# Performance work log

Measured on AMD Instinct MI355X. Metric: run time of the kernel, lower is better.

## Reference

```python
import jax, jax.numpy as jnp
import numpy as np

B, T, HID, OUT = 32, 2048, 1024, 1024
DV = 1024
NEG_INF = jnp.float32(-jnp.inf)


def setup_inputs() -> dict:
    key = jax.random.key(0)
    ks = jax.random.split(key, 10)
    hidden = jax.random.normal(ks[0], (B, HID), dtype=jnp.float32)
    enc_key = jax.random.normal(ks[1], (B, T, OUT), dtype=jnp.float32)
    value = jax.random.normal(ks[2], (B, T, DV), dtype=jnp.float32)
    seq_lens = jnp.maximum(jax.random.randint(ks[3], (B,), 0, T), 1).astype(jnp.int32)
    # learned parameters (PyTorch Linear: y = x @ W.T + b; we store W already transposed)
    s_q = 1.0 / np.sqrt(HID)
    s_1 = 1.0 / np.sqrt(OUT)
    s_2 = 1.0 / np.sqrt(OUT // 2)
    Wq = jax.random.uniform(ks[4], (HID, OUT), minval=-s_q, maxval=s_q, dtype=jnp.float32)
    bq = jax.random.uniform(ks[5], (OUT,), minval=-s_q, maxval=s_q, dtype=jnp.float32)
    W1 = jax.random.uniform(ks[6], (OUT, OUT // 2), minval=-s_1, maxval=s_1, dtype=jnp.float32)
    b1 = jax.random.uniform(ks[7], (OUT // 2,), minval=-s_1, maxval=s_1, dtype=jnp.float32)
    W2 = jax.random.uniform(ks[8], (OUT // 2, 1), minval=-s_2, maxval=s_2, dtype=jnp.float32)
    b2 = jax.random.uniform(ks[9], (1,), minval=-s_2, maxval=s_2, dtype=jnp.float32)
    return {"hidden": hidden, "key": enc_key, "value": value, "seq_lens": seq_lens,
            "Wq": Wq, "bq": bq, "W1": W1, "b1": b1, "W2": W2, "b2": b2}


def reference(hidden, key, value, seq_lens, Wq, bq, W1, b1, W2, b2):
    # query projection: [B, OUT]
    query = hidden @ Wq + bq
    # additive Bahdanau: tanh(key + query) -> [B, T, OUT]
    h = jnp.tanh(key + query[:, None, :])
    # 2-layer score MLP (dropout p=0.2 is identity in eval mode)
    h = h @ W1 + b1                      # [B, T, OUT//2]
    scores = (h @ W2 + b2)[..., 0]       # [B, T]
    # mask positions >= seq_len with -inf, then softmax over T
    pos = jnp.arange(scores.shape[1])
    scores = jnp.where(pos[None, :] < seq_lens[:, None], scores, NEG_INF)
    attn = jax.nn.softmax(scores, axis=-1)  # [B, T]
    # context = attn @ value -> [B, DV]
    context = jnp.einsum('bt,btd->bd', attn, value)
    return (context, attn)
```

## Files before the change

### kernel.cpp

```cpp
#include <hip/hip_runtime.h>
#include <math.h>

#define BB 32
#define TT 2048
#define DD 1024
#define HF 512

#define QKS 64
#define QCH (DD / QKS)

#define CHK 32
#define NCH (TT / CHK)

__device__ __forceinline__ float tanh_fast(float x) {
    float e = __expf(2.0f * x);
    return 1.0f - 2.0f / (e + 1.0f);
}

__global__ void __launch_bounds__(256) prep_query_kernel(
        const float* __restrict__ hidden, const float* __restrict__ Wq,
        const float* __restrict__ W1, const float* __restrict__ b1,
        const float* __restrict__ W2, const float* __restrict__ b2,
        float* __restrict__ w, float* __restrict__ cbias,
        float* __restrict__ qpart) {
    __shared__ float smem[BB * QCH];
    int bx  = blockIdx.x;
    int tid = threadIdx.x;

    if (bx < 4) {
        int d = bx * 256 + tid;
        const float* row = W1 + (size_t)d * HF;
        float acc = 0.0f;
        #pragma unroll 8
        for (int j = 0; j < HF; j += 4) {
            float4 a = *(const float4*)(row + j);
            float4 b = *(const float4*)(W2 + j);
            acc += a.x * b.x + a.y * b.y + a.z * b.z + a.w * b.w;
        }
        w[d] = acc;
        return;
    }
    if (bx == 4) {
        __shared__ float red[256];
        float s = b1[tid] * W2[tid] + b1[tid + 256] * W2[tid + 256];
        red[tid] = s;
        __syncthreads();
        for (int off = 128; off; off >>= 1) {
            if (tid < off) red[tid] += red[tid + off];
            __syncthreads();
        }
        if (tid == 0) cbias[0] = red[0] + b2[0];
        return;
    }
    int idx = bx - 5, otile = idx & 3, ks = idx >> 2;
    int o = otile * 256 + tid, h0 = ks * QCH;
    if (tid < 128) {
        int r = tid >> 2, c4 = (tid & 3) << 2;
        *(float4*)&smem[r * QCH + c4] = *(const float4*)&hidden[(size_t)r * DD + h0 + c4];
    }
    __syncthreads();

    float wv[QCH];
    #pragma unroll
    for (int h = 0; h < QCH; ++h)
        wv[h] = Wq[(size_t)(h0 + h) * DD + o];

    float acc[BB];
    #pragma unroll
    for (int b = 0; b < BB; ++b) acc[b] = 0.0f;
    #pragma unroll
    for (int h = 0; h < QCH; ++h) {
        #pragma unroll
        for (int b = 0; b < BB; ++b)
            acc[b] = fmaf(smem[b * QCH + h], wv[h], acc[b]);
    }
    #pragma unroll
    for (int b = 0; b < BB; ++b)
        qpart[((size_t)ks * BB + b) * DD + o] = acc[b];
}

__global__ void __launch_bounds__(256) qreduce_kernel(
        const float* __restrict__ qpart, const float* __restrict__ bq,
        float* __restrict__ query) {
    int i = blockIdx.x * 256 + threadIdx.x;
    int o = i & (DD - 1);
    float a0 = bq[o], a1 = 0.0f, a2 = 0.0f, a3 = 0.0f;
    #pragma unroll 4
    for (int ks = 0; ks < QKS; ks += 4) {
        a0 += qpart[(size_t)(ks + 0) * (BB * DD) + i];
        a1 += qpart[(size_t)(ks + 1) * (BB * DD) + i];
        a2 += qpart[(size_t)(ks + 2) * (BB * DD) + i];
        a3 += qpart[(size_t)(ks + 3) * (BB * DD) + i];
    }
    query[i] = (a0 + a1) + (a2 + a3);
}

__global__ void __launch_bounds__(256, 8) score_ctx_kernel(
        const float* __restrict__ key, const float* __restrict__ value,
        const float* __restrict__ query, const float* __restrict__ w,
        const float* __restrict__ cb, const int* __restrict__ seq_lens,
        float* __restrict__ escore, float* __restrict__ psum,
        float* __restrict__ partial) {
    int item = blockIdx.x;
    int b    = item & (BB - 1);
    int x    = item >> 5;
    int len  = seq_lens[b];
    int t0   = x * CHK;
    if (t0 >= len) return;

    __shared__ float wsh[DD];
    __shared__ float qsh[DD];
    __shared__ float esm[CHK];
    int tid = threadIdx.x;
    { int i4 = tid * 4;
      *(float4*)&wsh[i4] = *(const float4*)&w[i4];
      *(float4*)&qsh[i4] = *(const float4*)&query[(size_t)b * DD + i4]; }
    __syncthreads();

    int wave = tid >> 6, lane = tid & 63;
    float c0 = cb[0];

    #pragma unroll 4
    for (int tt = 0; tt < CHK / 4; ++tt) {
        int r = tt * 4 + wave;
        int t = t0 + r;
        float e = 0.0f;
        if (t < len) {
            const float* krow = key + ((size_t)b * TT + t) * DD;
            float acc = 0.0f;
            #pragma unroll
            for (int kb = 0; kb < 4; ++kb) {
                int d = kb * 256 + lane * 4;
                float4 kv = *(const float4*)(krow + d);
                float4 qv = *(const float4*)&qsh[d];
                float4 wv = *(const float4*)&wsh[d];
                acc += tanh_fast(kv.x + qv.x) * wv.x;
                acc += tanh_fast(kv.y + qv.y) * wv.y;
                acc += tanh_fast(kv.z + qv.z) * wv.z;
                acc += tanh_fast(kv.w + qv.w) * wv.w;
            }
            #pragma unroll
            for (int off = 32; off; off >>= 1) acc += __shfl_down(acc, off);
            if (lane == 0) e = __expf(acc + c0);
        }
        if (lane == 0) esm[r] = e;
    }
    __syncthreads();

    if (tid < CHK) escore[(size_t)b * TT + t0 + tid] = esm[tid];
    if (tid == 0) {
        float s = 0.0f;
        #pragma unroll
        for (int i = 0; i < CHK; ++i) s += esm[i];
        psum[b * NCH + x] = s;
    }

    int d4 = tid * 4;
    int tend = min(t0 + CHK, len);
    const float* vbase = value + (size_t)b * TT * DD + d4;
    float4 acc0 = {0.0f, 0.0f, 0.0f, 0.0f};
    float4 acc1 = {0.0f, 0.0f, 0.0f, 0.0f};
    int t = t0;
    for (; t + 1 < tend; t += 2) {
        float a0 = esm[t - t0], a1 = esm[t - t0 + 1];
        float4 v0 = *(const float4*)(vbase + (size_t)t * DD);
        float4 v1 = *(const float4*)(vbase + (size_t)(t + 1) * DD);
        acc0.x = fmaf(a0, v0.x, acc0.x);  acc1.x = fmaf(a1, v1.x, acc1.x);
        acc0.y = fmaf(a0, v0.y, acc0.y);  acc1.y = fmaf(a1, v1.y, acc1.y);
        acc0.z = fmaf(a0, v0.z, acc0.z);  acc1.z = fmaf(a1, v1.z, acc1.z);
        acc0.w = fmaf(a0, v0.w, acc0.w);  acc1.w = fmaf(a1, v1.w, acc1.w);
    }
    if (t < tend) {
        float a0 = esm[t - t0];
        float4 v0 = *(const float4*)(vbase + (size_t)t * DD);
        acc0.x = fmaf(a0, v0.x, acc0.x);
        acc0.y = fmaf(a0, v0.y, acc0.y);
        acc0.z = fmaf(a0, v0.z, acc0.z);
        acc0.w = fmaf(a0, v0.w, acc0.w);
    }
    acc0.x += acc1.x; acc0.y += acc1.y; acc0.z += acc1.z; acc0.w += acc1.w;
    *(float4*)&partial[((size_t)(b * NCH + x)) * DD + d4] = acc0;
}

__global__ void __launch_bounds__(256) finalize_kernel(
        const float* __restrict__ partial, const float* __restrict__ escore,
        const float* __restrict__ psum, const int* __restrict__ seq_lens,
        float* __restrict__ ctx, float* __restrict__ attn) {
    __shared__ float red[NCH];
    int bx = blockIdx.x, tid = threadIdx.x;
    int b  = (bx < 128) ? (bx >> 2) : (((bx - 128) * 1024) >> 11);
    int len = seq_lens[b];
    int nch = (len + CHK - 1) / CHK;

    if (tid < NCH) red[tid] = (tid < nch) ? psum[b * NCH + tid] : 0.0f;
    __syncthreads();
    for (int off = NCH / 2; off; off >>= 1) {
        if (tid < off) red[tid] += red[tid + off];
        __syncthreads();
    }
    float Sinv = 1.0f / red[0];

    if (bx < 128) {
        int d = (bx & 3) * 256 + tid;
        const float* pb = partial + (size_t)b * NCH * DD + d;
        float a0 = 0.0f, a1 = 0.0f, a2 = 0.0f, a3 = 0.0f;
        int c = 0;
        for (; c + 3 < nch; c += 4) {
            a0 += pb[(size_t)(c + 0) * DD];
            a1 += pb[(size_t)(c + 1) * DD];
            a2 += pb[(size_t)(c + 2) * DD];
            a3 += pb[(size_t)(c + 3) * DD];
        }
        for (; c < nch; ++c) a0 += pb[(size_t)c * DD];
        ctx[(size_t)b * DD + d] = ((a0 + a1) + (a2 + a3)) * Sinv;
    } else {
        int idx = (bx - 128) * 1024 + tid * 4;
        int t   = idx & (TT - 1);
        float4 e = *(const float4*)&escore[(size_t)b * TT + t];
        float4 o;
        o.x = (t + 0 < len) ? e.x * Sinv : 0.0f;
        o.y = (t + 1 < len) ? e.y * Sinv : 0.0f;
        o.z = (t + 2 < len) ? e.z * Sinv : 0.0f;
        o.w = (t + 3 < len) ? e.w * Sinv : 0.0f;
        *(float4*)&attn[(size_t)b * TT + t] = o;
    }
}

extern "C" void kernel_launch(void* const* d_in, const int* in_sizes, int n_in,
                              void* d_out, int out_size, void* d_ws, size_t ws_size,
                              hipStream_t stream) {
    const float* hidden   = (const float*)d_in[0];
    const float* key      = (const float*)d_in[1];
    const float* value    = (const float*)d_in[2];
    const int*   seq_lens = (const int*)  d_in[3];
    const float* Wq       = (const float*)d_in[4];
    const float* bq       = (const float*)d_in[5];
    const float* W1       = (const float*)d_in[6];
    const float* b1       = (const float*)d_in[7];
    const float* W2       = (const float*)d_in[8];
    const float* b2       = (const float*)d_in[9];

    float* out  = (float*)d_out;
    float* ctx  = out;
    float* attn = out + BB * DD;

    float* ws      = (float*)d_ws;
    float* w       = ws;
    float* cb      = ws + 1024;
    float* query   = ws + 2048;
    float* qpart   = query + BB * DD;
    float* escore  = qpart + (size_t)QKS * BB * DD;
    float* psum    = escore + BB * TT;
    float* partial = psum + BB * NCH;

    prep_query_kernel<<<dim3(5 + 4 * QKS), dim3(256), 0, stream>>>(
        hidden, Wq, W1, b1, W2, b2, w, cb, qpart);
    qreduce_kernel<<<dim3(BB * DD / 256), dim3(256), 0, stream>>>(qpart, bq, query);
    score_ctx_kernel<<<dim3(BB * NCH), dim3(256), 0, stream>>>(
        key, value, query, w, cb, seq_lens, escore, psum, partial);
    finalize_kernel<<<dim3(192), dim3(256), 0, stream>>>(
        partial, escore, psum, seq_lens, ctx, attn);
}
```

Before: 95.43 us.

## Double-buffer key loads, unroll value loop, and split reductions across thread groups

In the score kernel, the next key row is now prefetched into a register double buffer while tanh runs on the current row. Occupancy is relaxed from 8 to 6 blocks per CU to make room for those registers. The value accumulation now uses four independent accumulators and always covers the full chunk, relying on zeroed scores past the sequence length. This trades some wasted value loads on each sequence's last chunk for more loads in flight. Separately, the query reduction and the finalize context reduction are split across two thread groups with a shared-memory combine, using more blocks, and tanh uses a hardware reciprocal instead of a divide.

```diff
diff --git a/kernel.cpp b/kernel.cpp
--- a/kernel.cpp
+++ b/kernel.cpp
@@ -14,7 +14,7 @@
 
 __device__ __forceinline__ float tanh_fast(float x) {
     float e = __expf(2.0f * x);
-    return 1.0f - 2.0f / (e + 1.0f);
+    return 1.0f - 2.0f * __builtin_amdgcn_rcpf(e + 1.0f);
 }
 
 __global__ void __launch_bounds__(256) prep_query_kernel(
@@ -82,20 +82,26 @@
 __global__ void __launch_bounds__(256) qreduce_kernel(
         const float* __restrict__ qpart, const float* __restrict__ bq,
         float* __restrict__ query) {
-    int i = blockIdx.x * 256 + threadIdx.x;
-    int o = i & (DD - 1);
-    float a0 = bq[o], a1 = 0.0f, a2 = 0.0f, a3 = 0.0f;
-    #pragma unroll 4
-    for (int ks = 0; ks < QKS; ks += 4) {
-        a0 += qpart[(size_t)(ks + 0) * (BB * DD) + i];
-        a1 += qpart[(size_t)(ks + 1) * (BB * DD) + i];
-        a2 += qpart[(size_t)(ks + 2) * (BB * DD) + i];
-        a3 += qpart[(size_t)(ks + 3) * (BB * DD) + i];
-    }
-    query[i] = (a0 + a1) + (a2 + a3);
-}
-
-__global__ void __launch_bounds__(256, 8) score_ctx_kernel(
+    __shared__ float part[256];
+    int bx = blockIdx.x, tid = threadIdx.x;
+    int e = tid & 127, g = tid >> 7;
+    int i = bx * 128 + e;
+    int ks0 = g * (QKS / 2);
+    float a0 = 0.0f, a1 = 0.0f, a2 = 0.0f, a3 = 0.0f;
+    #pragma unroll 8
+    for (int k = 0; k < QKS / 2; k += 4) {
+        size_t base = (size_t)(ks0 + k) * (BB * DD) + i;
+        a0 += qpart[base];
+        a1 += qpart[base + (size_t)(BB * DD)];
+        a2 += qpart[base + 2 * (size_t)(BB * DD)];
+        a3 += qpart[base + 3 * (size_t)(BB * DD)];
+    }
+    part[tid] = (a0 + a1) + (a2 + a3);
+    __syncthreads();
+    if (g == 0) query[i] = bq[i & (DD - 1)] + part[tid] + part[tid + 128];
+}
+
+__global__ void __launch_bounds__(256, 6) score_ctx_kernel(
         const float* __restrict__ key, const float* __restrict__ value,
         const float* __restrict__ query, const float* __restrict__ w,
         const float* __restrict__ cb, const int* __restrict__ seq_lens,
@@ -119,31 +125,43 @@
 
     int wave = tid >> 6, lane = tid & 63;
     float c0 = cb[0];
-
-    #pragma unroll 4
-    for (int tt = 0; tt < CHK / 4; ++tt) {
-        int r = tt * 4 + wave;
-        int t = t0 + r;
-        float e = 0.0f;
-        if (t < len) {
-            const float* krow = key + ((size_t)b * TT + t) * DD;
-            float acc = 0.0f;
+    const float* kb0 = key + (size_t)b * TT * DD;
+
+    float4 kreg[2][4];
+    {
+        int t = min(t0 + wave, len - 1);
+        const float* kr = kb0 + (size_t)t * DD;
+        #pragma unroll
+        for (int s = 0; s < 4; ++s)
+            kreg[0][s] = *(const float4*)(kr + s * 256 + lane * 4);
+    }
+    #pragma unroll
+    for (int j = 0; j < 8; ++j) {
+        if (j < 7) {
+            int t = min(t0 + (j + 1) * 4 + wave, len - 1);
+            const float* kr = kb0 + (size_t)t * DD;
             #pragma unroll
-            for (int kb = 0; kb < 4; ++kb) {
-                int d = kb * 256 + lane * 4;
-                float4 kv = *(const float4*)(krow + d);
-                float4 qv = *(const float4*)&qsh[d];
-                float4 wv = *(const float4*)&wsh[d];
-                acc += tanh_fast(kv.x + qv.x) * wv.x;
-                acc += tanh_fast(kv.y + qv.y) * wv.y;
-                acc += tanh_fast(kv.z + qv.z) * wv.z;
-                acc += tanh_fast(kv.w + qv.w) * wv.w;
-            }
-            #pragma unroll
-            for (int off = 32; off; off >>= 1) acc += __shfl_down(acc, off);
-            if (lane == 0) e = __expf(acc + c0);
-        }
-        if (lane == 0) esm[r] = e;
+            for (int s = 0; s < 4; ++s)
+                kreg[(j + 1) & 1][s] = *(const float4*)(kr + s * 256 + lane * 4);
+        }
+        float acc = 0.0f;
+        #pragma unroll
+        for (int s = 0; s < 4; ++s) {
+            int d = s * 256 + lane * 4;
+            float4 kv = kreg[j & 1][s];
+            float4 qv = *(const float4*)&qsh[d];
+            float4 wv = *(const float4*)&wsh[d];
+            acc += tanh_fast(kv.x + qv.x) * wv.x;
+            acc += tanh_fast(kv.y + qv.y) * wv.y;
+            acc += tanh_fast(kv.z + qv.z) * wv.z;
+            acc += tanh_fast(kv.w + qv.w) * wv.w;
+        }
+        #pragma unroll
+        for (int off = 32; off; off >>= 1) acc += __shfl_down(acc, off);
+        if (lane == 0) {
+            int t = t0 + j * 4 + wave;
+            esm[j * 4 + wave] = (t < len) ? __expf(acc + c0) : 0.0f;
+        }
     }
     __syncthreads();
 
@@ -156,30 +174,31 @@
     }
 
     int d4 = tid * 4;
-    int tend = min(t0 + CHK, len);
     const float* vbase = value + (size_t)b * TT * DD + d4;
-    float4 acc0 = {0.0f, 0.0f, 0.0f, 0.0f};
-    float4 acc1 = {0.0f, 0.0f, 0.0f, 0.0f};
-    int t = t0;
-    for (; t + 1 < tend; t += 2) {
-        float a0 = esm[t - t0], a1 = esm[t - t0 + 1];
-        float4 v0 = *(const float4*)(vbase + (size_t)t * DD);
-        float4 v1 = *(const float4*)(vbase + (size_t)(t + 1) * DD);
-        acc0.x = fmaf(a0, v0.x, acc0.x);  acc1.x = fmaf(a1, v1.x, acc1.x);
-        acc0.y = fmaf(a0, v0.y, acc0.y);  acc1.y = fmaf(a1, v1.y, acc1.y);
-        acc0.z = fmaf(a0, v0.z, acc0.z);  acc1.z = fmaf(a1, v1.z, acc1.z);
-        acc0.w = fmaf(a0, v0.w, acc0.w);  acc1.w = fmaf(a1, v1.w, acc1.w);
-    }
-    if (t < tend) {
-        float a0 = esm[t - t0];
-        float4 v0 = *(const float4*)(vbase + (size_t)t * DD);
-        acc0.x = fmaf(a0, v0.x, acc0.x);
-        acc0.y = fmaf(a0, v0.y, acc0.y);
-        acc0.z = fmaf(a0, v0.z, acc0.z);
-        acc0.w = fmaf(a0, v0.w, acc0.w);
-    }
-    acc0.x += acc1.x; acc0.y += acc1.y; acc0.z += acc1.z; acc0.w += acc1.w;
-    *(float4*)&partial[((size_t)(b * NCH + x)) * DD + d4] = acc0;
+    float4 A0 = {0.0f, 0.0f, 0.0f, 0.0f};
+    float4 A1 = A0, A2 = A0, A3 = A0;
+    #pragma unroll 2
+    for (int tt = 0; tt < CHK; tt += 4) {
+        float e0 = esm[tt], e1 = esm[tt + 1], e2 = esm[tt + 2], e3 = esm[tt + 3];
+        float4 v0 = *(const float4*)(vbase + (size_t)(t0 + tt    ) * DD);
+        float4 v1 = *(const float4*)(vbase + (size_t)(t0 + tt + 1) * DD);
+        float4 v2 = *(const float4*)(vbase + (size_t)(t0 + tt + 2) * DD);
+        float4 v3 = *(const float4*)(vbase + (size_t)(t0 + tt + 3) * DD);
+        A0.x = fmaf(e0, v0.x, A0.x); A0.y = fmaf(e0, v0.y, A0.y);
+        A0.z = fmaf(e0, v0.z, A0.z); A0.w = fmaf(e0, v0.w, A0.w);
+        A1.x = fmaf(e1, v1.x, A1.x); A1.y = fmaf(e1, v1.y, A1.y);
+        A1.z = fmaf(e1, v1.z, A1.z); A1.w = fmaf(e1, v1.w, A1.w);
+        A2.x = fmaf(e2, v2.x, A2.x); A2.y = fmaf(e2, v2.y, A2.y);
+        A2.z = fmaf(e2, v2.z, A2.z); A2.w = fmaf(e2, v2.w, A2.w);
+        A3.x = fmaf(e3, v3.x, A3.x); A3.y = fmaf(e3, v3.y, A3.y);
+        A3.z = fmaf(e3, v3.z, A3.z); A3.w = fmaf(e3, v3.w, A3.w);
+    }
+    float4 R;
+    R.x = (A0.x + A1.x) + (A2.x + A3.x);
+    R.y = (A0.y + A1.y) + (A2.y + A3.y);
+    R.z = (A0.z + A1.z) + (A2.z + A3.z);
+    R.w = (A0.w + A1.w) + (A2.w + A3.w);
+    *(float4*)&partial[((size_t)(b * NCH + x)) * DD + d4] = R;
 }
 
 __global__ void __launch_bounds__(256) finalize_kernel(
@@ -187,41 +206,47 @@
         const float* __restrict__ psum, const int* __restrict__ seq_lens,
         float* __restrict__ ctx, float* __restrict__ attn) {
     __shared__ float red[NCH];
+    __shared__ float part[256];
     int bx = blockIdx.x, tid = threadIdx.x;
-    int b  = (bx < 128) ? (bx >> 2) : (((bx - 128) * 1024) >> 11);
+    int b  = (bx < 256) ? (bx >> 3) : ((bx - 256) >> 1);
     int len = seq_lens[b];
     int nch = (len + CHK - 1) / CHK;
 
     if (tid < NCH) red[tid] = (tid < nch) ? psum[b * NCH + tid] : 0.0f;
     __syncthreads();
+    #pragma unroll
     for (int off = NCH / 2; off; off >>= 1) {
         if (tid < off) red[tid] += red[tid + off];
         __syncthreads();
     }
     float Sinv = 1.0f / red[0];
 
-    if (bx < 128) {
-        int d = (bx & 3) * 256 + tid;
+    if (bx < 256) {
+        int e = tid & 127, g = tid >> 7;
+        int d = (bx & 7) * 128 + e;
         const float* pb = partial + (size_t)b * NCH * DD + d;
+        int cbeg = g * 32, cend = min(nch, cbeg + 32);
         float a0 = 0.0f, a1 = 0.0f, a2 = 0.0f, a3 = 0.0f;
-        int c = 0;
-        for (; c + 3 < nch; c += 4) {
+        int c = cbeg;
+        for (; c + 3 < cend; c += 4) {
             a0 += pb[(size_t)(c + 0) * DD];
             a1 += pb[(size_t)(c + 1) * DD];
             a2 += pb[(size_t)(c + 2) * DD];
             a3 += pb[(size_t)(c + 3) * DD];
         }
-        for (; c < nch; ++c) a0 += pb[(size_t)c * DD];
-        ctx[(size_t)b * DD + d] = ((a0 + a1) + (a2 + a3)) * Sinv;
+        for (; c < cend; ++c) a0 += pb[(size_t)c * DD];
+        part[tid] = (a0 + a1) + (a2 + a3);
+        __syncthreads();
+        if (g == 0) ctx[(size_t)b * DD + d] = (part[tid] + part[tid + 128]) * Sinv;
     } else {
-        int idx = (bx - 128) * 1024 + tid * 4;
+        int idx = (bx - 256) * 1024 + tid * 4;
         int t   = idx & (TT - 1);
-        float4 e = *(const float4*)&escore[(size_t)b * TT + t];
+        float4 e4 = *(const float4*)&escore[(size_t)b * TT + t];
         float4 o;
-        o.x = (t + 0 < len) ? e.x * Sinv : 0.0f;
-        o.y = (t + 1 < len) ? e.y * Sinv : 0.0f;
-        o.z = (t + 2 < len) ? e.z * Sinv : 0.0f;
-        o.w = (t + 3 < len) ? e.w * Sinv : 0.0f;
+        o.x = (t + 0 < len) ? e4.x * Sinv : 0.0f;
+        o.y = (t + 1 < len) ? e4.y * Sinv : 0.0f;
+        o.z = (t + 2 < len) ? e4.z * Sinv : 0.0f;
+        o.w = (t + 3 < len) ? e4.w * Sinv : 0.0f;
         *(float4*)&attn[(size_t)b * TT + t] = o;
     }
 }
@@ -255,9 +280,9 @@
 
     prep_query_kernel<<<dim3(5 + 4 * QKS), dim3(256), 0, stream>>>(
         hidden, Wq, W1, b1, W2, b2, w, cb, qpart);
-    qreduce_kernel<<<dim3(BB * DD / 256), dim3(256), 0, stream>>>(qpart, bq, query);
+    qreduce_kernel<<<dim3(BB * DD / 128), dim3(256), 0, stream>>>(qpart, bq, query);
     score_ctx_kernel<<<dim3(BB * NCH), dim3(256), 0, stream>>>(
         key, value, query, w, cb, seq_lens, escore, psum, partial);
-    finalize_kernel<<<dim3(192), dim3(256), 0, stream>>>(
+    finalize_kernel<<<dim3(320), dim3(256), 0, stream>>>(
         partial, escore, psum, seq_lens, ctx, attn);
 }
```

Result: faster. 85.36 us (-10.5%).
